# Kernel optimization log

Hardware: AMD Instinct MI355X
Metric: run time of the kernel (lower is better)

## Reference

```python
import jax, jax.numpy as jnp
import numpy as np

N, C, T, V = 16, 64, 512, 25
R, O, S = 8, 64, 3  # rel_channels, out_channels, num_subset


def setup_inputs() -> dict:
    key = jax.random.key(0)
    ks = jax.random.split(key, 12)
    sc = 0.05
    return {
        "x": jax.random.normal(ks[0], (N, C, T, V), jnp.float32),
        "A": jax.random.normal(ks[1], (S, V, V), jnp.float32) * 0.1,
        "alpha": jax.random.normal(ks[2], (1,), jnp.float32) * 0.1,
        "w1": jax.random.normal(ks[3], (S, R, C), jnp.float32) * sc,
        "b1": jax.random.normal(ks[4], (S, R), jnp.float32) * sc,
        "w2": jax.random.normal(ks[5], (S, R, C), jnp.float32) * sc,
        "b2": jax.random.normal(ks[6], (S, R), jnp.float32) * sc,
        "w3": jax.random.normal(ks[7], (S, O, C), jnp.float32) * sc,
        "b3": jax.random.normal(ks[8], (S, O), jnp.float32) * sc,
        "w4": jax.random.normal(ks[9], (S, O, R), jnp.float32) * sc,
        "b4": jax.random.normal(ks[10], (S, O), jnp.float32) * sc,
        "sparse": 0,
    }


def _mask(w, thr):
    # SparseConv2d: magnitude-threshold the 1x1 conv weights at runtime.
    return jnp.where(jnp.abs(w) > thr, w, jnp.zeros_like(w))


def reference(x, A, alpha, w1, b1, w2, b2, w3, b3, w4, b4, sparse):
    thr = jnp.float32(sparse)

    def conv1x1(w, b, inp):  # w [o,c], b [o], inp [n,c,t,v] -> [n,o,t,v]
        return jnp.einsum('oc,nctv->notv', _mask(w, thr), inp) + b[None, :, None, None]

    y = None
    for i in range(A.shape[0]):
        x1 = conv1x1(w1[i], b1[i], x).mean(-2)          # [n,r,v]
        x2 = conv1x1(w2[i], b2[i], x).mean(-2)          # [n,r,v]
        x3 = conv1x1(w3[i], b3[i], x)                   # [n,o,t,v]
        att = jnp.tanh(x1[..., :, None] - x2[..., None, :])  # [n,r,v,v]
        a = jnp.einsum('or,nruv->nouv', _mask(w4[i], thr), att) + b4[i][None, :, None, None]
        a = a * alpha + A[i][None, None]                # [n,o,v,v]
        z = jnp.einsum('ncuv,nctu->nctv', a, x3)        # node aggregation
        y = z if y is None else y + z
    # in_channels == out_channels -> residual is identity
    return jax.nn.relu(y + x)
```

## Files before the change

### kernel.cpp

```cpp
#include <hip/hip_runtime.h>
#include <cmath>

typedef __bf16 bf16x4v __attribute__((ext_vector_type(4)));
typedef __bf16 bf16x8 __attribute__((ext_vector_type(8)));
typedef float f32x4 __attribute__((ext_vector_type(4)));

namespace {
constexpr int kN = 16, kC = 64, kT = 512, kV = 25, kS = 3, kO = 64;
constexpr int kTV = kT * kV;
constexpr size_t WS_AFRAG = 102400;
constexpr size_t WS_W3F = WS_AFRAG + (size_t)48 * 131072;
constexpr size_t WS_XBF = WS_W3F + 3 * 8192;
}

__device__ __forceinline__ int swzB16(int c, int t, int ubyte) {
  return (c << 10) + (((t << 6) + ubyte) ^ ((((c ^ t) & 7)) << 4));
}

__global__ __launch_bounds__(256) void k1_cvt(const float* __restrict__ x,
                                              __bf16* __restrict__ xbf,
                                              float* __restrict__ xm) {
  const int bid = blockIdx.x;
  __shared__ float part[250][4];
  const int tid = threadIdx.x;
  const float4* xg4 = (const float4*)(x + (size_t)bid * kTV);
  bf16x4v* xb4 = (bf16x4v*)(xbf + (size_t)bid * kTV);
  if (tid < 250) {
    float a0 = 0.f, a1 = 0.f, a2 = 0.f, a3 = 0.f;
    for (int j = tid; j < 3200; j += 250) {
      float4 v = xg4[j];
      a0 += v.x; a1 += v.y; a2 += v.z; a3 += v.w;
      bf16x4v o;
      o[0] = (__bf16)v.x; o[1] = (__bf16)v.y;
      o[2] = (__bf16)v.z; o[3] = (__bf16)v.w;
      xb4[j] = o;
    }
    part[tid][0] = a0; part[tid][1] = a1; part[tid][2] = a2; part[tid][3] = a3;
  }
  __syncthreads();
  if (tid < 25) {
    float s = 0.f;
#pragma unroll
    for (int r = 0; r < 4; ++r) {
      int q = ((tid - r + 25) % 25) * 19 % 25;
#pragma unroll
      for (int p = 0; p < 10; ++p) s += part[q + 25 * p][r];
    }
    xm[bid * 25 + tid] = s * (1.f / 512.f);
  }
}

__global__ __launch_bounds__(256) void k2_attn(
    const float* __restrict__ xm, const float* __restrict__ Ag,
    const float* __restrict__ alpha, const float* __restrict__ w1,
    const float* __restrict__ b1, const float* __restrict__ w2,
    const float* __restrict__ b2, const float* __restrict__ w3,
    const float* __restrict__ w4, const float* __restrict__ b4,
    const int* __restrict__ sparse, unsigned char* __restrict__ ws) {
  const float thr = (float)sparse[0];
  const int b = blockIdx.x;
  const int s = b >> 6, n = (b >> 2) & 15, q = b & 3;
  __shared__ float xm_l[1600];
  __shared__ float x1_l[200], x2_l[200];
  __shared__ float att_l[8 * 625];
  __shared__ float attsum_l[200];
  __shared__ float ag_l[625];
  __shared__ float acs_l[25];
  __shared__ float w4_l[512];
  const int tid = threadIdx.x;
  for (int i = tid; i < 1600; i += 256) xm_l[i] = xm[n * 1600 + i];
  for (int i = tid; i < 512; i += 256) {
    float w = w4[s * 512 + i];
    w4_l[i] = (fabsf(w) > thr) ? w : 0.f;
  }
  for (int i = tid; i < 625; i += 256) ag_l[i] = Ag[s * 625 + i];
  __syncthreads();
  for (int i = tid; i < 400; i += 256) {
    int which = i / 200, idx = i % 200, r = idx / 25, u = idx % 25;
    const float* wrow = (which == 0 ? w1 : w2) + (s * 8 + r) * 64;
    float acc = 0.f;
    for (int cc = 0; cc < 64; ++cc) {
      float w = wrow[cc];
      w = (fabsf(w) > thr) ? w : 0.f;
      acc += w * xm_l[cc * 25 + u];
    }
    acc += (which == 0 ? b1 : b2)[s * 8 + r];
    if (which == 0) x1_l[idx] = acc;
    else x2_l[idx] = acc;
  }
  __syncthreads();
  for (int i = tid; i < 8 * 625; i += 256) {
    int r = i / 625, uv = i % 625, u = uv / 25, v = uv % 25;
    att_l[i] = tanhf(x1_l[r * 25 + u] - x2_l[r * 25 + v]);
  }
  __syncthreads();
  if (tid < 200) {
    int r = tid / 25, v = tid % 25;
    float sum = 0.f;
    for (int u = 0; u < 25; ++u) sum += att_l[r * 625 + u * 25 + v];
    attsum_l[tid] = sum;
  } else if (tid < 225) {
    int v = tid - 200;
    float sum = 0.f;
    for (int u = 0; u < 25; ++u) sum += ag_l[u * 25 + v];
    acs_l[v] = sum;
  }
  __syncthreads();
  const float al = alpha[0];
  unsigned char* afrag = ws + WS_AFRAG + (size_t)(s * 16 + n) * 131072;
  for (int slot = q * 2048 + tid; slot < (q + 1) * 2048; slot += 256) {
    int c = slot >> 7, vt = (slot >> 6) & 1, l = slot & 63;
    int v = vt * 16 + (l & 15), g = l >> 4;
    bf16x8 out;
    if (v < 25) {
      float b4v = b4[s * 64 + c];
#pragma unroll
      for (int j = 0; j < 8; ++j) {
        int u = g * 8 + j;
        float val = 0.f;
        if (u < 25) {
          float acc = 0.f;
#pragma unroll
          for (int r = 0; r < 8; ++r) acc += w4_l[c * 8 + r] * att_l[r * 625 + u * 25 + v];
          val = al * (acc + b4v) + ag_l[u * 25 + v];
        } else if (u == 25) {
          float acc = 0.f;
#pragma unroll
          for (int r = 0; r < 8; ++r) acc += w4_l[c * 8 + r] * attsum_l[r * 25 + v];
          val = al * acc + 25.f * al * b4v + acs_l[v];
        }
        out[j] = (__bf16)val;
      }
    } else {
#pragma unroll
      for (int j = 0; j < 8; ++j) out[j] = (__bf16)0.f;
    }
    *(bf16x8*)(afrag + (size_t)slot * 16) = out;
  }
  if (n == 0 && tid < 128) {
    unsigned char* w3f = ws + WS_W3F + (size_t)s * 8192;
    int slot = q * 128 + tid;
    int ot = slot >> 7, ks = (slot >> 6) & 1, l = slot & 63;
    int o = ot * 16 + (l & 15), g = l >> 4;
    bf16x8 out;
#pragma unroll
    for (int j = 0; j < 8; ++j) {
      int cp = ks * 32 + g * 8 + j;
      float w = w3[(s * 64 + o) * 64 + cp];
      out[j] = (__bf16)((fabsf(w) > thr) ? w : 0.f);
    }
    *(bf16x8*)(w3f + slot * 16) = out;
  }
}

__global__ __launch_bounds__(512) void k3_main(const __bf16* __restrict__ xbf,
                                               const float* __restrict__ b3,
                                               const unsigned char* __restrict__ ws,
                                               float* __restrict__ y) {
  const int n = blockIdx.x;
  const int tb = blockIdx.y;
  extern __shared__ __align__(16) unsigned char smem[];
  const int tid = threadIdx.x;
  const int w = tid >> 6, l = tid & 63, g = l >> 4, l15 = l & 15;

  for (int idx = tid; idx < 3072; idx += 512) {
    int pair = idx / 3, k = idx % 3;
    int c = pair >> 4, t = pair & 15;
    *(unsigned int*)(smem + swzB16(c, t, 52 + 4 * k)) = 0u;
  }

  bf16x8 xa[4][2];
#pragma unroll
  for (int cti = 0; cti < 4; ++cti)
#pragma unroll
    for (int kf = 0; kf < 2; ++kf)
#pragma unroll
      for (int j = 0; j < 8; ++j) xa[cti][kf][j] = (__bf16)0.f;
  {
    const __bf16* xbp = xbf + (size_t)n * kC * kTV;
#pragma unroll
    for (int cti = 0; cti < 4; ++cti) {
      int tt = tb * 16 + 2 * w + (cti >> 1);
      int u = (cti & 1) * 16 + l15;
      if (u < 25) {
#pragma unroll
        for (int kf = 0; kf < 2; ++kf)
#pragma unroll
          for (int j = 0; j < 8; ++j) {
            int cp = kf * 32 + g * 8 + j;
            xa[cti][kf][j] = xbp[(size_t)cp * kTV + tt * 25 + u];
          }
      }
    }
  }
  __syncthreads();

  const unsigned char* afrag = ws + WS_AFRAG;
  const unsigned char* w3f = ws + WS_W3F;

  f32x4 zacc[8][2];
#pragma unroll
  for (int cc = 0; cc < 8; ++cc)
#pragma unroll
    for (int vt = 0; vt < 2; ++vt) {
      f32x4 zz = {0.f, 0.f, 0.f, 0.f};
      zacc[cc][vt] = zz;
    }

  for (int s = 0; s < kS; ++s) {
    bf16x8 B2[8][2];
    const unsigned char* af = afrag + (size_t)(s * 16 + n) * 131072;
#pragma unroll
    for (int cc = 0; cc < 8; ++cc) {
      int c = w * 8 + cc;
#pragma unroll
      for (int vt = 0; vt < 2; ++vt)
        B2[cc][vt] = *(const bf16x8*)(af + ((c * 2 + vt) * 64 + l) * 16);
    }
    if (s) __syncthreads();

    const unsigned char* w3l = w3f + (size_t)s * 8192;
#pragma unroll
    for (int ot = 0; ot < 4; ++ot) {
      bf16x8 wk0 = *(const bf16x8*)(w3l + ((ot * 2 + 0) * 64 + l) * 16);
      bf16x8 wk1 = *(const bf16x8*)(w3l + ((ot * 2 + 1) * 64 + l) * 16);
      int c = ot * 16 + l15;
#pragma unroll
      for (int cti = 0; cti < 4; ++cti) {
        f32x4 d = {0.f, 0.f, 0.f, 0.f};
        d = __builtin_amdgcn_mfma_f32_16x16x32_bf16(xa[cti][0], wk0, d, 0, 0, 0);
        d = __builtin_amdgcn_mfma_f32_16x16x32_bf16(xa[cti][1], wk1, d, 0, 0, 0);
        int tt = 2 * w + (cti >> 1);
        if (!(cti & 1)) {
          bf16x4v pk;
          pk[0] = (__bf16)d[0]; pk[1] = (__bf16)d[1];
          pk[2] = (__bf16)d[2]; pk[3] = (__bf16)d[3];
          *(bf16x4v*)(smem + swzB16(c, tt, g * 8)) = pk;
        } else if (g < 2) {
          bf16x4v pk;
          pk[0] = (__bf16)d[0]; pk[1] = (__bf16)d[1];
          pk[2] = (__bf16)d[2]; pk[3] = (__bf16)d[3];
          *(bf16x4v*)(smem + swzB16(c, tt, 32 + g * 8)) = pk;
        } else if (g == 2) {
          *(__bf16*)(smem + swzB16(c, tt, 48)) = (__bf16)d[0];
        }
      }
    }
    for (int i = tid; i < 1024; i += 512) {
      int c = i >> 4, t = i & 15;
      *(__bf16*)(smem + swzB16(c, t, 50)) = (__bf16)b3[s * 64 + c];
    }
    __syncthreads();
#pragma unroll
    for (int cc = 0; cc < 8; ++cc) {
      int c = w * 8 + cc;
      bf16x8 a2 = *(const bf16x8*)(smem + swzB16(c, l15, g * 16));
      zacc[cc][0] = __builtin_amdgcn_mfma_f32_16x16x32_bf16(a2, B2[cc][0], zacc[cc][0], 0, 0, 0);
      zacc[cc][1] = __builtin_amdgcn_mfma_f32_16x16x32_bf16(a2, B2[cc][1], zacc[cc][1], 0, 0, 0);
    }
  }
  __syncthreads();
  float* zs = (float*)smem;
  const __bf16* xbp = xbf + (size_t)n * kC * kTV;
  float4* yg4 = (float4*)(y + (size_t)n * kC * kTV);
#pragma unroll
  for (int h = 0; h < 2; ++h) {
    if ((w >> 2) == h) {
      int c0l = (w & 3) * 8;
#pragma unroll
      for (int cc = 0; cc < 8; ++cc)
#pragma unroll
        for (int vt = 0; vt < 2; ++vt) {
          int v = vt * 16 + l15;
          if (v < 25) {
#pragma unroll
            for (int jj = 0; jj < 4; ++jj)
              zs[(c0l + cc) * 400 + (g * 4 + jj) * 25 + v] = zacc[cc][vt][jj];
          }
        }
    }
    __syncthreads();
    for (int i4 = tid; i4 < 3200; i4 += 512) {
      int cl = i4 / 100, r4 = i4 % 100, c = h * 32 + cl;
      bf16x4v xv = *(const bf16x4v*)(xbp + (size_t)c * kTV + tb * 400 + r4 * 4);
      f32x4 zv = *(const f32x4*)(zs + cl * 400 + r4 * 4);
      float4 o;
      o.x = fmaxf(zv[0] + (float)xv[0], 0.f);
      o.y = fmaxf(zv[1] + (float)xv[1], 0.f);
      o.z = fmaxf(zv[2] + (float)xv[2], 0.f);
      o.w = fmaxf(zv[3] + (float)xv[3], 0.f);
      yg4[c * 3200 + tb * 100 + r4] = o;
    }
    __syncthreads();
  }
}

extern "C" void kernel_launch(void* const* d_in, const int* in_sizes, int n_in,
                              void* d_out, int out_size, void* d_ws, size_t ws_size,
                              hipStream_t stream) {
  const float* x = (const float*)d_in[0];
  const float* Ag = (const float*)d_in[1];
  const float* alpha = (const float*)d_in[2];
  const float* w1 = (const float*)d_in[3];
  const float* b1 = (const float*)d_in[4];
  const float* w2 = (const float*)d_in[5];
  const float* b2 = (const float*)d_in[6];
  const float* w3 = (const float*)d_in[7];
  const float* b3 = (const float*)d_in[8];
  const float* w4 = (const float*)d_in[9];
  const float* b4 = (const float*)d_in[10];
  const int* sparse = (const int*)d_in[11];

  unsigned char* ws = (unsigned char*)d_ws;
  float* xm = (float*)ws;
  __bf16* xbf = (__bf16*)(ws + WS_XBF);
  float* y = (float*)d_out;

  hipFuncSetAttribute((const void*)k3_main,
                      hipFuncAttributeMaxDynamicSharedMemorySize, 65536);

  k1_cvt<<<kN * kC, 256, 0, stream>>>(x, xbf, xm);
  k2_attn<<<kS * kN * 4, 256, 0, stream>>>(xm, Ag, alpha, w1, b1, w2, b2, w3, w4,
                                           b4, sparse, ws);
  dim3 g3(kN, kT / 16);
  k3_main<<<g3, 512, 65536, stream>>>(xbf, b3, ws, y);
}
```

Baseline: 79.88 us.

## Split k3 output channels across 4 blocks with smaller smem and threads

The main kernel now gets a third grid dimension that splits the 64 output channels into 4 groups of 16. Each block runs 256 threads, uses 25.6KB of dynamic shared memory, and computes x3 only for its own channel slice. The aim is more blocks and better occupancy, plus removing the two-pass epilogue and the large shared-memory attribute. In exchange, each block reloads the full 64-channel x tile from global memory once per subset, so input reads rise about 12x and the loads sit inside the s-loop.

```diff
diff --git a/kernel.cpp b/kernel.cpp
--- a/kernel.cpp
+++ b/kernel.cpp
@@ -13,7 +13,7 @@
 constexpr size_t WS_XBF = WS_W3F + 3 * 8192;
 }
 
-__device__ __forceinline__ int swzB16(int c, int t, int ubyte) {
+__device__ __forceinline__ int swzC(int c, int t, int ubyte) {
   return (c << 10) + (((t << 6) + ubyte) ^ ((((c ^ t) & 7)) << 4));
 }
 
@@ -153,54 +153,30 @@
   }
 }
 
-__global__ __launch_bounds__(512) void k3_main(const __bf16* __restrict__ xbf,
+__global__ __launch_bounds__(256) void k3_main(const __bf16* __restrict__ xbf,
                                                const float* __restrict__ b3,
                                                const unsigned char* __restrict__ ws,
                                                float* __restrict__ y) {
   const int n = blockIdx.x;
   const int tb = blockIdx.y;
+  const int h = blockIdx.z;
   extern __shared__ __align__(16) unsigned char smem[];
   const int tid = threadIdx.x;
   const int w = tid >> 6, l = tid & 63, g = l >> 4, l15 = l & 15;
 
-  for (int idx = tid; idx < 3072; idx += 512) {
+  for (int idx = tid; idx < 768; idx += 256) {
     int pair = idx / 3, k = idx % 3;
     int c = pair >> 4, t = pair & 15;
-    *(unsigned int*)(smem + swzB16(c, t, 52 + 4 * k)) = 0u;
-  }
-
-  bf16x8 xa[4][2];
-#pragma unroll
-  for (int cti = 0; cti < 4; ++cti)
-#pragma unroll
-    for (int kf = 0; kf < 2; ++kf)
-#pragma unroll
-      for (int j = 0; j < 8; ++j) xa[cti][kf][j] = (__bf16)0.f;
-  {
-    const __bf16* xbp = xbf + (size_t)n * kC * kTV;
-#pragma unroll
-    for (int cti = 0; cti < 4; ++cti) {
-      int tt = tb * 16 + 2 * w + (cti >> 1);
-      int u = (cti & 1) * 16 + l15;
-      if (u < 25) {
-#pragma unroll
-        for (int kf = 0; kf < 2; ++kf)
-#pragma unroll
-          for (int j = 0; j < 8; ++j) {
-            int cp = kf * 32 + g * 8 + j;
-            xa[cti][kf][j] = xbp[(size_t)cp * kTV + tt * 25 + u];
-          }
-      }
-    }
-  }
-  __syncthreads();
-
+    *(unsigned int*)(smem + swzC(c, t, 52 + 4 * k)) = 0u;
+  }
+
+  const __bf16* xbp = xbf + (size_t)n * kC * kTV;
   const unsigned char* afrag = ws + WS_AFRAG;
   const unsigned char* w3f = ws + WS_W3F;
 
-  f32x4 zacc[8][2];
-#pragma unroll
-  for (int cc = 0; cc < 8; ++cc)
+  f32x4 zacc[4][2];
+#pragma unroll
+  for (int cc = 0; cc < 4; ++cc)
 #pragma unroll
     for (int vt = 0; vt < 2; ++vt) {
       f32x4 zz = {0.f, 0.f, 0.f, 0.f};
@@ -208,90 +184,93 @@
     }
 
   for (int s = 0; s < kS; ++s) {
-    bf16x8 B2[8][2];
+    bf16x8 B2[4][2];
     const unsigned char* af = afrag + (size_t)(s * 16 + n) * 131072;
 #pragma unroll
-    for (int cc = 0; cc < 8; ++cc) {
-      int c = w * 8 + cc;
+    for (int cc = 0; cc < 4; ++cc) {
+      int cg = h * 16 + w * 4 + cc;
 #pragma unroll
       for (int vt = 0; vt < 2; ++vt)
-        B2[cc][vt] = *(const bf16x8*)(af + ((c * 2 + vt) * 64 + l) * 16);
-    }
+        B2[cc][vt] = *(const bf16x8*)(af + ((cg * 2 + vt) * 64 + l) * 16);
+    }
+    const unsigned char* w3l = w3f + (size_t)s * 8192;
+    bf16x8 wk0 = *(const bf16x8*)(w3l + ((h * 2 + 0) * 64 + l) * 16);
+    bf16x8 wk1 = *(const bf16x8*)(w3l + ((h * 2 + 1) * 64 + l) * 16);
     if (s) __syncthreads();
 
-    const unsigned char* w3l = w3f + (size_t)s * 8192;
-#pragma unroll
-    for (int ot = 0; ot < 4; ++ot) {
-      bf16x8 wk0 = *(const bf16x8*)(w3l + ((ot * 2 + 0) * 64 + l) * 16);
-      bf16x8 wk1 = *(const bf16x8*)(w3l + ((ot * 2 + 1) * 64 + l) * 16);
-      int c = ot * 16 + l15;
-#pragma unroll
-      for (int cti = 0; cti < 4; ++cti) {
-        f32x4 d = {0.f, 0.f, 0.f, 0.f};
-        d = __builtin_amdgcn_mfma_f32_16x16x32_bf16(xa[cti][0], wk0, d, 0, 0, 0);
-        d = __builtin_amdgcn_mfma_f32_16x16x32_bf16(xa[cti][1], wk1, d, 0, 0, 0);
-        int tt = 2 * w + (cti >> 1);
-        if (!(cti & 1)) {
-          bf16x4v pk;
-          pk[0] = (__bf16)d[0]; pk[1] = (__bf16)d[1];
-          pk[2] = (__bf16)d[2]; pk[3] = (__bf16)d[3];
-          *(bf16x4v*)(smem + swzB16(c, tt, g * 8)) = pk;
-        } else if (g < 2) {
-          bf16x4v pk;
-          pk[0] = (__bf16)d[0]; pk[1] = (__bf16)d[1];
-          pk[2] = (__bf16)d[2]; pk[3] = (__bf16)d[3];
-          *(bf16x4v*)(smem + swzB16(c, tt, 32 + g * 8)) = pk;
-        } else if (g == 2) {
-          *(__bf16*)(smem + swzB16(c, tt, 48)) = (__bf16)d[0];
+#pragma unroll
+    for (int i = 0; i < 8; ++i) {
+      int tl = i >> 1, uh = i & 1;
+      int t = w * 4 + tl;
+      int tt = tb * 16 + t;
+      int u = uh * 16 + l15;
+      bf16x8 xa0, xa1;
+#pragma unroll
+      for (int j = 0; j < 8; ++j) { xa0[j] = (__bf16)0.f; xa1[j] = (__bf16)0.f; }
+      if (u < 25) {
+#pragma unroll
+        for (int j = 0; j < 8; ++j) {
+          int cp = g * 8 + j;
+          xa0[j] = xbp[(size_t)cp * kTV + tt * 25 + u];
+          xa1[j] = xbp[(size_t)(cp + 32) * kTV + tt * 25 + u];
         }
       }
-    }
-    for (int i = tid; i < 1024; i += 512) {
-      int c = i >> 4, t = i & 15;
-      *(__bf16*)(smem + swzB16(c, t, 50)) = (__bf16)b3[s * 64 + c];
-    }
+      f32x4 d = {0.f, 0.f, 0.f, 0.f};
+      d = __builtin_amdgcn_mfma_f32_16x16x32_bf16(xa0, wk0, d, 0, 0, 0);
+      d = __builtin_amdgcn_mfma_f32_16x16x32_bf16(xa1, wk1, d, 0, 0, 0);
+      if (uh == 0) {
+        bf16x4v pk;
+        pk[0] = (__bf16)d[0]; pk[1] = (__bf16)d[1];
+        pk[2] = (__bf16)d[2]; pk[3] = (__bf16)d[3];
+        *(bf16x4v*)(smem + swzC(l15, t, g * 8)) = pk;
+      } else if (g < 2) {
+        bf16x4v pk;
+        pk[0] = (__bf16)d[0]; pk[1] = (__bf16)d[1];
+        pk[2] = (__bf16)d[2]; pk[3] = (__bf16)d[3];
+        *(bf16x4v*)(smem + swzC(l15, t, 32 + g * 8)) = pk;
+      } else if (g == 2) {
+        *(__bf16*)(smem + swzC(l15, t, 48)) = (__bf16)d[0];
+      }
+    }
+    *(__bf16*)(smem + swzC(tid >> 4, tid & 15, 50)) =
+        (__bf16)b3[s * 64 + h * 16 + (tid >> 4)];
     __syncthreads();
 #pragma unroll
-    for (int cc = 0; cc < 8; ++cc) {
-      int c = w * 8 + cc;
-      bf16x8 a2 = *(const bf16x8*)(smem + swzB16(c, l15, g * 16));
+    for (int cc = 0; cc < 4; ++cc) {
+      int c = w * 4 + cc;
+      bf16x8 a2 = *(const bf16x8*)(smem + swzC(c, l15, g * 16));
       zacc[cc][0] = __builtin_amdgcn_mfma_f32_16x16x32_bf16(a2, B2[cc][0], zacc[cc][0], 0, 0, 0);
       zacc[cc][1] = __builtin_amdgcn_mfma_f32_16x16x32_bf16(a2, B2[cc][1], zacc[cc][1], 0, 0, 0);
     }
   }
   __syncthreads();
   float* zs = (float*)smem;
-  const __bf16* xbp = xbf + (size_t)n * kC * kTV;
+#pragma unroll
+  for (int cc = 0; cc < 4; ++cc) {
+    int c = w * 4 + cc;
+#pragma unroll
+    for (int vt = 0; vt < 2; ++vt) {
+      int v = vt * 16 + l15;
+      if (v < 25) {
+#pragma unroll
+        for (int jj = 0; jj < 4; ++jj)
+          zs[c * 400 + (g * 4 + jj) * 25 + v] = zacc[cc][vt][jj];
+      }
+    }
+  }
+  __syncthreads();
   float4* yg4 = (float4*)(y + (size_t)n * kC * kTV);
-#pragma unroll
-  for (int h = 0; h < 2; ++h) {
-    if ((w >> 2) == h) {
-      int c0l = (w & 3) * 8;
-#pragma unroll
-      for (int cc = 0; cc < 8; ++cc)
-#pragma unroll
-        for (int vt = 0; vt < 2; ++vt) {
-          int v = vt * 16 + l15;
-          if (v < 25) {
-#pragma unroll
-            for (int jj = 0; jj < 4; ++jj)
-              zs[(c0l + cc) * 400 + (g * 4 + jj) * 25 + v] = zacc[cc][vt][jj];
-          }
-        }
-    }
-    __syncthreads();
-    for (int i4 = tid; i4 < 3200; i4 += 512) {
-      int cl = i4 / 100, r4 = i4 % 100, c = h * 32 + cl;
-      bf16x4v xv = *(const bf16x4v*)(xbp + (size_t)c * kTV + tb * 400 + r4 * 4);
-      f32x4 zv = *(const f32x4*)(zs + cl * 400 + r4 * 4);
-      float4 o;
-      o.x = fmaxf(zv[0] + (float)xv[0], 0.f);
-      o.y = fmaxf(zv[1] + (float)xv[1], 0.f);
-      o.z = fmaxf(zv[2] + (float)xv[2], 0.f);
-      o.w = fmaxf(zv[3] + (float)xv[3], 0.f);
-      yg4[c * 3200 + tb * 100 + r4] = o;
-    }
-    __syncthreads();
+  for (int i4 = tid; i4 < 1600; i4 += 256) {
+    int cl = i4 / 100, r4 = i4 % 100;
+    int cg = h * 16 + cl;
+    bf16x4v xv = *(const bf16x4v*)(xbp + (size_t)cg * kTV + tb * 400 + r4 * 4);
+    f32x4 zv = *(const f32x4*)(zs + cl * 400 + r4 * 4);
+    float4 o;
+    o.x = fmaxf(zv[0] + (float)xv[0], 0.f);
+    o.y = fmaxf(zv[1] + (float)xv[1], 0.f);
+    o.z = fmaxf(zv[2] + (float)xv[2], 0.f);
+    o.w = fmaxf(zv[3] + (float)xv[3], 0.f);
+    yg4[cg * 3200 + tb * 100 + r4] = o;
   }
 }
 
@@ -316,12 +295,9 @@
   __bf16* xbf = (__bf16*)(ws + WS_XBF);
   float* y = (float*)d_out;
 
-  hipFuncSetAttribute((const void*)k3_main,
-                      hipFuncAttributeMaxDynamicSharedMemorySize, 65536);
-
   k1_cvt<<<kN * kC, 256, 0, stream>>>(x, xbf, xm);
   k2_attn<<<kS * kN * 4, 256, 0, stream>>>(xm, Ag, alpha, w1, b1, w2, b2, w3, w4,
                                            b4, sparse, ws);
-  dim3 g3(kN, kT / 16);
-  k3_main<<<g3, 512, 65536, stream>>>(xbf, b3, ws, y);
-}
+  dim3 g3(kN, kT / 16, 4);
+  k3_main<<<g3, 256, 25600, stream>>>(xbf, b3, ws, y);
+}
```

After: 118.5 us. +48.4%, slower.
